# Kernel tuning notes

Measured on AMD Instinct MI355X. Metric: run time of the kernel, lower is better.

## Reference

```python
import jax, jax.numpy as jnp
import numpy as np

KD = 128   # scratch_keys_dim
NP = 3     # n_pointers
STEPS = 3  # max_program_steps


def _gru_cell(x, h, w_ih, w_hh, b_ih, b_hh):
    # torch.nn.GRUCell math
    gi = x @ w_ih.T + b_ih            # [B, 3H]
    gh = h @ w_hh.T + b_hh            # [B, 3H]
    ir, iz, inn = jnp.split(gi, 3, axis=-1)
    hr, hz, hn = jnp.split(gh, 3, axis=-1)
    r = jax.nn.sigmoid(ir + hr)
    z = jax.nn.sigmoid(iz + hz)
    n = jnp.tanh(inn + r * hn)
    return (1.0 - z) * n + z * h


def setup_inputs() -> dict:
    key = jax.random.key(0)
    ks = jax.random.split(key, 9)
    B, Lw, La, V, P, H = 256, 12, 51, 1000, 200, 3 * KD
    instructions = jax.random.randint(ks[0], (Lw, B), 0, V)
    true_actions = jax.random.randint(ks[1], (La, B), 0, V)
    gate_emb = jax.random.normal(ks[2], (V, 2)) * 0.1
    program_emb = jax.random.normal(ks[3], (V, P)) * 0.1
    primitive_emb = jax.random.normal(ks[4], (V, V)) * 0.1
    # sinusoidal positional encoding = scratch_keys buffer
    pos = np.arange(50)[:, None].astype(np.float32)
    div = np.exp(np.arange(0, KD, 2).astype(np.float32) * (-np.log(10000.0) / KD))
    pe = np.zeros((50, KD), np.float32)
    pe[:, 0::2] = np.sin(pos * div)
    pe[:, 1::2] = np.cos(pos * div)
    scratch_keys = jnp.asarray(pe)
    init_value = jnp.zeros((V,), jnp.float32).at[0].set(1.0)  # one-hot at eos_idx=0
    w_ih = jax.random.normal(ks[5], (3 * H, P)) * 0.05
    w_hh = jax.random.normal(ks[6], (3 * H, H)) * 0.05
    b_ih = jax.random.normal(ks[7], (3 * H,)) * 0.05
    b_hh = jax.random.normal(ks[8], (3 * H,)) * 0.05
    return dict(gate_emb=gate_emb, program_emb=program_emb, primitive_emb=primitive_emb,
                scratch_keys=scratch_keys, init_value=init_value,
                w_ih=w_ih, w_hh=w_hh, b_ih=b_ih, b_hh=b_hh,
                instructions=instructions, true_actions=true_actions)


def reference(gate_emb, program_emb, primitive_emb, scratch_keys, init_value,
              w_ih, w_hh, b_ih, b_hh, instructions, true_actions):
    ins = instructions[1:-1]          # drop BOS/EOS, [Lw-2, B]
    acts = true_actions[1:]           # [L, B]
    L = acts.shape[0]                 # scratch length (50)
    B = instructions.shape[1]
    V = init_value.shape[0]
    keys = scratch_keys[:L]           # [L, KD]
    h0 = jnp.tile(scratch_keys[0], (B, NP))           # [B, 3*KD]
    sv0 = jnp.tile(init_value, (B, L, 1))             # [B, L, V]

    def word_step(carry, word):
        h, sv = carry
        gate = jax.nn.softmax(gate_emb[word], axis=-1)     # [B, 2]
        program = program_emb[word]                        # [B, P]
        primitive = primitive_emb[word]                    # [B, V]
        g0 = gate[:, 0:1]
        g1 = gate[:, 1:2]
        for _ in range(STEPS):
            read_p = h[:, KD:2 * KD]
            write_p = h[:, 2 * KD:3 * KD]
            # attention read from scratch memory
            read_attn = jax.nn.softmax(read_p @ keys.T, axis=-1)      # [B, L]
            read_value = jnp.einsum('bl,blv->bv', read_attn, sv)       # [B, V]
            # gated mix of primitive embedding and read value
            new_value = g0 * primitive + g1 * read_value                # [B, V]
            # attention write
            write_mask = jax.nn.softmax(write_p @ keys.T, axis=-1)      # [B, L]
            wm = write_mask[..., None]                                  # [B, L, 1]
            sv = wm * new_value[:, None, :] + (1.0 - wm) * sv
            # gated GRU controller update
            h_new = _gru_cell(program, h, w_ih, w_hh, b_ih, b_hh)
            h = g0 * h + g1 * h_new
        return (h, sv), None

    (_, sv), _ = jax.lax.scan(word_step, (h0, sv0), ins)
    actions = jax.nn.log_softmax(sv, axis=-1)          # [B, L, V]
    actions = jnp.transpose(actions, (0, 2, 1))        # [B, V, L]
    return actions, acts.T                             # ([B,V,L], [B,L])
```

## Files before the change

### kernel.cpp

```cpp
#include <hip/hip_runtime.h>
#include <hip/hip_fp16.h>
#include <hip/hip_fp8.h>

#define B_ 256
#define V_ 1000
#define P_ 200
#define L_ 50
#define H_ 384
#define H3_ 1152
#define NW_ 10
#define OUT1_OFF 12800000

typedef _Float16 half8 __attribute__((ext_vector_type(8)));
typedef _Float16 half4_t __attribute__((ext_vector_type(4)));
typedef _Float16 half2_t __attribute__((ext_vector_type(2)));
typedef float floatx4 __attribute__((ext_vector_type(4)));

__global__ __launch_bounds__(256) void prep_kernel(
    const float* __restrict__ gate_emb, const float* __restrict__ prog_emb,
    const float* __restrict__ w_ih, const float* __restrict__ w_hh,
    const int* __restrict__ instr, const int* __restrict__ tacts,
    float* __restrict__ g01, unsigned char* __restrict__ whhP,
    unsigned char* __restrict__ whhR,
    _Float16* __restrict__ wih_h, _Float16* __restrict__ prog_h,
    float* __restrict__ out)
{
  const int stride = gridDim.x * blockDim.x;
  const int tid = blockIdx.x * blockDim.x + threadIdx.x;

  for (int i = tid; i < 147456; i += stride) {
    const int e = i & 7, p = (i >> 3) & 1, l = (i >> 4) & 63;
    const int q = i >> 10;
    const int u = q % 18, w = q / 18;
    const int g = u / 6, kap = u - 6*g;
    const int kc = 2*kap + p;
    const int row = g*384 + 48*w + 16*2 + (l & 15);
    const int col = kc*32 + (l >> 4)*8 + e;
    __hip_fp8_e4m3 qv(w_hh[row*H_ + col]);
    whhP[i] = qv.__x;
  }
  for (int i = tid; i < 294912; i += stride) {
    const int e = i & 7, p = (i >> 3) & 1, l = (i >> 4) & 63;
    const int q = i >> 10;
    const int u = q % 36, w = q / 36;
    const int j = u / 18, rem = u - 18*j;
    const int g = rem / 6, kap = rem - 6*g;
    const int kc = 2*kap + p;
    const int row = g*384 + 48*w + 16*j + (l & 15);
    const int col = kc*32 + (l >> 4)*8 + e;
    __hip_fp8_e4m3 qv(w_hh[row*H_ + col]);
    whhR[i] = qv.__x;
  }
  for (int i = tid; i < H3_*224; i += stride) {
    int r = i / 224, c = i - r*224;
    wih_h[i] = (_Float16)(c < P_ ? w_ih[r*P_ + c] : 0.f);
  }
  for (int i = tid; i < V_*P_; i += stride) prog_h[i] = (_Float16)prog_emb[i];
  for (int i = tid; i < NW_*B_; i += stride) {
    int w = i / B_, b = i - w*B_;
    int word = instr[(1+w)*B_ + b];
    float e0 = gate_emb[word*2], e1 = gate_emb[word*2+1];
    float m = fmaxf(e0, e1);
    float a = __expf(e0-m), c = __expf(e1-m);
    float inv = 1.f/(a+c);
    g01[i*2] = a*inv; g01[i*2+1] = c*inv;
  }
  for (int i = tid; i < B_*L_; i += stride) {
    int b = i / L_, l = i - b*L_;
    out[OUT1_OFF + i] = (float)tacts[(1+l)*B_ + b];
  }
}

__global__ __launch_bounds__(256) void gi_gemm(
    const _Float16* __restrict__ prog_h, const _Float16* __restrict__ wih_h,
    const float* __restrict__ b_ih, const float* __restrict__ b_hh,
    float* __restrict__ giv)
{
  __shared__ _Float16 pA[16][232];
  const int tid = threadIdx.x;
  const int v0 = blockIdx.x * 16;
  const int n0 = blockIdx.y * 64;

  for (int i = tid; i < 16*224; i += 256) {
    int r = i / 224, c = i - r*224;
    int v = v0 + r;
    _Float16 val = (_Float16)0.f;
    if (v < V_ && c < P_) val = prog_h[v*P_ + c];
    pA[r][c] = val;
  }
  __syncthreads();

  const int wave = tid >> 6, lane = tid & 63;
  const int m = lane & 15, kg = lane >> 4;
  const int n_t = n0 + wave*16;
  floatx4 acc = {0.f, 0.f, 0.f, 0.f};
  #pragma unroll
  for (int ks = 0; ks < 7; ++ks) {
    const int kk = ks*32 + kg*8;
    half8 av = *(const half8*)&pA[m][kk];
    half8 bv = *(const half8*)&wih_h[(n_t + m)*224 + kk];
    acc = __builtin_amdgcn_mfma_f32_16x16x32_f16(av, bv, acc, 0, 0, 0);
  }
  const int nn = n_t + m;
  const float bias = b_ih[nn] + (nn < 768 ? b_hh[nn] : 0.f);
  #pragma unroll
  for (int r = 0; r < 4; ++r) {
    int mm = v0 + kg*4 + r;
    if (mm < V_) giv[(size_t)mm*H3_ + nn] = acc[r] + bias;
  }
}

__global__ __launch_bounds__(512, 2) void steps_kernel(
    const uint4* __restrict__ whhPp, const uint4* __restrict__ whhRp,
    const float* __restrict__ giv, const float* __restrict__ g01,
    const float* __restrict__ keys, const float* __restrict__ bhh,
    const int* __restrict__ instr, _Float16* __restrict__ hdump)
{
  __shared__ uint4 ldsP[9216];
  __shared__ unsigned long long hA[768];

  const int bid = blockIdx.x, b0 = bid*16, tid = threadIdx.x;
  const int w = tid >> 6, lane = tid & 63, m_ = lane & 15, kg = lane >> 4;

  for (int i = tid; i < 9216; i += 512) ldsP[i] = whhPp[i];

  const uint4* __restrict__ rbase = whhRp + (size_t)w*36*64 + lane;

  float hreg[3][4];
  float bbn[3];
  half2_t gvh[18];
  float g0r[4], g1r[4];

  #pragma unroll
  for (int j = 0; j < 3; ++j) bbn[j] = bhh[768 + 48*w + 16*j + m_];

  #pragma unroll
  for (int j = 0; j < 3; ++j) {
    const float h0 = keys[(48*w + 16*j + m_) & 127];
    #pragma unroll
    for (int r = 0; r < 4; ++r) hreg[j][r] = h0;
  }

  #pragma unroll
  for (int j = 0; j < 3; ++j) {
    const int c = 48*w + 16*j + m_;
    const int base = (c >> 5)*512 + ((c >> 3) & 3)*128 + (c & 7);
    half4_t hv;
    #pragma unroll
    for (int r = 0; r < 4; ++r) {
      __hip_fp8_e4m3 q(hreg[j][r]);
      ((unsigned char*)hA)[base + (kg*4 + r)*8] = q.__x;
      hv[r] = (_Float16)hreg[j][r];
    }
    *(half4_t*)&hdump[(((size_t)0*16 + bid)*384 + c)*16 + kg*4] = hv;
  }

  {
    int4 wd4 = *(const int4*)&instr[(1+0)*B_ + b0 + kg*4];
    int wdr[4] = {wd4.x, wd4.y, wd4.z, wd4.w};
    #pragma unroll
    for (int r = 0; r < 4; ++r) {
      float2 gg = *(const float2*)&g01[(size_t)(b0 + kg*4 + r)*2];
      g0r[r] = gg.x; g1r[r] = gg.y;
    }
    #pragma unroll
    for (int r = 0; r < 4; ++r) {
      const float* gp = giv + (size_t)wdr[r]*H3_;
      #pragma unroll
      for (int j = 0; j < 3; ++j)
        #pragma unroll
        for (int g = 0; g < 3; ++g) {
          const int f = r*9 + j*3 + g;
          gvh[f >> 1][f & 1] = (_Float16)gp[g*384 + 48*w + 16*j + m_];
        }
    }
  }

  uint4 W00 = rbase[ 0*64], W01 = rbase[ 1*64], W02 = rbase[ 2*64];
  uint4 W03 = rbase[ 3*64], W04 = rbase[ 4*64], W05 = rbase[ 5*64];
  uint4 W06 = rbase[ 6*64], W07 = rbase[ 7*64], W08 = rbase[ 8*64];
  uint4 W09 = rbase[ 9*64], W10 = rbase[10*64], W11 = rbase[11*64];
  uint4 W12 = rbase[12*64], W13 = rbase[13*64], W14 = rbase[14*64];
  uint4 W15 = rbase[15*64], W16 = rbase[16*64], W17 = rbase[17*64];
  uint4 W18 = rbase[18*64], W19 = rbase[19*64], W20 = rbase[20*64];
  uint4 W21 = rbase[21*64], W22 = rbase[22*64], W23 = rbase[23*64];
  uint4 W24 = rbase[24*64], W25 = rbase[25*64], W26 = rbase[26*64];
  uint4 W27 = rbase[27*64], W28 = rbase[28*64], W29 = rbase[29*64];
  uint4 W30 = rbase[30*64], W31 = rbase[31*64], W32 = rbase[32*64];
  uint4 W33 = rbase[33*64], W34 = rbase[34*64], W35 = rbase[35*64];

#define PIN4(W) asm volatile("" : "+v"(W.x), "+v"(W.y), "+v"(W.z), "+v"(W.w))
  PIN4(W00); PIN4(W01); PIN4(W02); PIN4(W03); PIN4(W04); PIN4(W05);
  PIN4(W06); PIN4(W07); PIN4(W08); PIN4(W09); PIN4(W10); PIN4(W11);
  PIN4(W12); PIN4(W13); PIN4(W14); PIN4(W15); PIN4(W16); PIN4(W17);
  PIN4(W18); PIN4(W19); PIN4(W20); PIN4(W21); PIN4(W22); PIN4(W23);
  PIN4(W24); PIN4(W25); PIN4(W26); PIN4(W27); PIN4(W28); PIN4(W29);
  PIN4(W30); PIN4(W31); PIN4(W32); PIN4(W33); PIN4(W34); PIN4(W35);
#undef PIN4

  asm volatile("s_waitcnt lgkmcnt(0)\n\ts_barrier" ::: "memory");

#define LO64(W) ((long)((((unsigned long long)(W).y) << 32) | (W).x))
#define HI64(W) ((long)((((unsigned long long)(W).w) << 32) | (W).z))
#define GVF(F) ((float)gvh[(F) >> 1][(F) & 1])
#define KSTEP(KAP, WA, WB, WC) \
  a0 = hA[(2*(KAP))*64 + lane]; a1 = hA[(2*(KAP)+1)*64 + lane]; \
  acc0 = __builtin_amdgcn_mfma_f32_16x16x32_fp8_fp8((long)a0, LO64(WA), acc0, 0, 0, 0); \
  acc0 = __builtin_amdgcn_mfma_f32_16x16x32_fp8_fp8((long)a1, HI64(WA), acc0, 0, 0, 0); \
  acc1 = __builtin_amdgcn_mfma_f32_16x16x32_fp8_fp8((long)a0, LO64(WB), acc1, 0, 0, 0); \
  acc1 = __builtin_amdgcn_mfma_f32_16x16x32_fp8_fp8((long)a1, HI64(WB), acc1, 0, 0, 0); \
  acc2 = __builtin_amdgcn_mfma_f32_16x16x32_fp8_fp8((long)a0, LO64(WC), acc2, 0, 0, 0); \
  acc2 = __builtin_amdgcn_mfma_f32_16x16x32_fp8_fp8((long)a1, HI64(WC), acc2, 0, 0, 0);
#define KSTEPL(KAP) \
  { a0 = hA[(2*(KAP))*64 + lane]; a1 = hA[(2*(KAP)+1)*64 + lane]; \
    uint4 P0 = ldsP[(w*18 +      (KAP))*64 + lane]; \
    uint4 P1 = ldsP[(w*18 +  6 + (KAP))*64 + lane]; \
    uint4 P2 = ldsP[(w*18 + 12 + (KAP))*64 + lane]; \
    acc0 = __builtin_amdgcn_mfma_f32_16x16x32_fp8_fp8((long)a0, LO64(P0), acc0, 0, 0, 0); \
    acc0 = __builtin_amdgcn_mfma_f32_16x16x32_fp8_fp8((long)a1, HI64(P0), acc0, 0, 0, 0); \
    acc1 = __builtin_amdgcn_mfma_f32_16x16x32_fp8_fp8((long)a0, LO64(P1), acc1, 0, 0, 0); \
    acc1 = __builtin_amdgcn_mfma_f32_16x16x32_fp8_fp8((long)a1, HI64(P1), acc1, 0, 0, 0); \
    acc2 = __builtin_amdgcn_mfma_f32_16x16x32_fp8_fp8((long)a0, LO64(P2), acc2, 0, 0, 0); \
    acc2 = __builtin_amdgcn_mfma_f32_16x16x32_fp8_fp8((long)a1, HI64(P2), acc2, 0, 0, 0); }
#define EPI(J) \
  _Pragma("unroll") \
  for (int r = 0; r < 4; ++r) { \
    const float rg = 1.f/(1.f + __expf(-(GVF(r*9+(J)*3+0) + acc0[r]))); \
    const float z  = 1.f/(1.f + __expf(-(GVF(r*9+(J)*3+1) + acc1[r]))); \
    const float x2 = GVF(r*9+(J)*3+2) + rg*(acc2[r] + bbn[(J)]); \
    const float nn = 2.f/(1.f + __expf(-2.f*x2)) - 1.f; \
    const float hold = hreg[(J)][r]; \
    const float hnew = (1.f - z)*nn + z*hold; \
    hreg[(J)][r] = g0r[r]*hold + g1r[r]*hnew; \
  }

  #pragma unroll 1
  for (int t = 0; t < 30; ++t) {
    unsigned long long a0, a1;
    floatx4 acc0, acc1, acc2;

    acc0 = (floatx4){0.f,0.f,0.f,0.f}; acc1 = acc0; acc2 = acc0;
    KSTEP(0, W00, W06, W12) KSTEP(1, W01, W07, W13) KSTEP(2, W02, W08, W14)
    KSTEP(3, W03, W09, W15) KSTEP(4, W04, W10, W16) KSTEP(5, W05, W11, W17)
    EPI(0)
    acc0 = (floatx4){0.f,0.f,0.f,0.f}; acc1 = acc0; acc2 = acc0;
    KSTEP(0, W18, W24, W30) KSTEP(1, W19, W25, W31) KSTEP(2, W20, W26, W32)
    KSTEP(3, W21, W27, W33) KSTEP(4, W22, W28, W34) KSTEP(5, W23, W29, W35)
    EPI(1)
    acc0 = (floatx4){0.f,0.f,0.f,0.f}; acc1 = acc0; acc2 = acc0;
    KSTEPL(0) KSTEPL(1) KSTEPL(2) KSTEPL(3) KSTEPL(4) KSTEPL(5)
    EPI(2)

    asm volatile("s_waitcnt lgkmcnt(0)\n\ts_barrier" ::: "memory");

    #pragma unroll
    for (int j = 0; j < 3; ++j) {
      const int c = 48*w + 16*j + m_;
      const int base = (c >> 5)*512 + ((c >> 3) & 3)*128 + (c & 7);
      half4_t hv;
      #pragma unroll
      for (int r = 0; r < 4; ++r) {
        __hip_fp8_e4m3 q(hreg[j][r]);
        ((unsigned char*)hA)[base + (kg*4 + r)*8] = q.__x;
        hv[r] = (_Float16)hreg[j][r];
      }
      *(half4_t*)&hdump[(((size_t)(t+1)*16 + bid)*384 + c)*16 + kg*4] = hv;
    }

    if (t % 3 == 2) {
      const int wi = (t/3 + 1 < 10) ? t/3 + 1 : 9;
      int4 wd4 = *(const int4*)&instr[(1+wi)*B_ + b0 + kg*4];
      int wdr[4] = {wd4.x, wd4.y, wd4.z, wd4.w};
      #pragma unroll
      for (int r = 0; r < 4; ++r) {
        float2 gg = *(const float2*)&g01[((size_t)wi*B_ + b0 + kg*4 + r)*2];
        g0r[r] = gg.x; g1r[r] = gg.y;
      }
      #pragma unroll
      for (int r = 0; r < 4; ++r) {
        const float* gp = giv + (size_t)wdr[r]*H3_;
        #pragma unroll
        for (int j = 0; j < 3; ++j)
          #pragma unroll
          for (int g = 0; g < 3; ++g) {
            const int f = r*9 + j*3 + g;
            gvh[f >> 1][f & 1] = (_Float16)gp[g*384 + 48*w + 16*j + m_];
          }
      }
    }

    asm volatile("s_waitcnt lgkmcnt(0)\n\ts_barrier" ::: "memory");
  }
  asm volatile("s_waitcnt vmcnt(0) lgkmcnt(0)" ::: "memory");
#undef KSTEP
#undef KSTEPL
#undef EPI
#undef GVF
#undef LO64
#undef HI64
}

__global__ __launch_bounds__(256) void attnS_kernel(
    const _Float16* __restrict__ hdump, const float* __restrict__ keys,
    const float* __restrict__ g01, float* __restrict__ S_buf)
{
  __shared__ float keysT[128][52];
  __shared__ float hT[30][256];
  __shared__ float sc[30][2][52];
  __shared__ float Sr[50][13];
  __shared__ float g0a[10], g1a[10];
  __shared__ float nvs[12];

  const int b = blockIdx.x, g = b >> 4, bl = b & 15;
  const int tid = threadIdx.x, wv = tid >> 6, lane = tid & 63;

  for (int i = tid; i < 128*L_; i += 256) {
    int k = i / L_, l = i - k*L_;
    keysT[k][l] = keys[l*128 + k];
  }
  for (int i = tid; i < 30*256; i += 256) {
    int t = i >> 8, c = i & 255;
    hT[t][c] = (float)hdump[(((size_t)t*16 + g)*384 + 128 + c)*16 + bl];
  }
  for (int i = tid; i < 550; i += 256) Sr[i/11][i%11] = ((i % 11) == 0) ? 1.f : 0.f;
  if (tid < NW_) {
    float2 gg = *(const float2*)&g01[((size_t)tid*B_ + b)*2];
    g0a[tid] = gg.x; g1a[tid] = gg.y;
  }
  __syncthreads();

  for (int row = wv; row < 60; row += 4) {
    const int t = row >> 1, ty = row & 1;
    float s = 0.f;
    if (lane < L_) {
      #pragma unroll 8
      for (int k = 0; k < 128; ++k)
        s += hT[t][ty*128 + k] * keysT[k][lane];
    }
    float val = (lane < L_) ? s : -1e30f;
    float mx = val;
    #pragma unroll
    for (int off = 32; off; off >>= 1) mx = fmaxf(mx, __shfl_xor(mx, off));
    float e = (lane < L_) ? __expf(val - mx) : 0.f;
    float sm = e;
    #pragma unroll
    for (int off = 32; off; off >>= 1) sm += __shfl_xor(sm, off);
    if (lane < L_) sc[t][ty][lane] = e / sm;
  }
  __syncthreads();

  for (int t = 0; t < 30; ++t) {
    const int widx = t / 3;
    if (tid < 11) {
      float rv = 0.f;
      #pragma unroll 5
      for (int l = 0; l < L_; ++l) rv += sc[t][0][l] * Sr[l][tid];
      nvs[tid] = g1a[widx]*rv + ((tid == 1 + widx) ? g0a[widx] : 0.f);
    }
    __syncthreads();
    for (int i = tid; i < 550; i += 256) {
      const int l = i / 11, j = i - l*11;
      const float wm = sc[t][1][l];
      Sr[l][j] = wm*nvs[j] + (1.f - wm)*Sr[l][j];
    }
    __syncthreads();
  }

  for (int i = tid; i < 550; i += 256) {
    const int l = i / 11, j = i - l*11;
    S_buf[(size_t)b*600 + l*12 + j] = Sr[l][j];
  }
}

__global__ __launch_bounds__(512) void epi_kernel(
    const float* __restrict__ S_buf, const float* __restrict__ prim_emb,
    const float* __restrict__ iv_g, const int* __restrict__ instr,
    float* __restrict__ out)
{
  __shared__ float prim[10][1000];
  __shared__ float iv[1000];
  __shared__ float SrT[11][52];
  __shared__ float lss[52];
  __shared__ int wds[10];

  const int b = blockIdx.x;
  const int tid = threadIdx.x;

  if (tid < 10) wds[tid] = instr[(1+tid)*B_ + b];
  for (int i = tid; i < 550; i += 512) {
    int l = i / 11, j = i - l*11;
    SrT[j][l] = S_buf[(size_t)b*600 + l*12 + j];
  }
  for (int i = tid; i < 250; i += 512) ((float4*)iv)[i] = ((const float4*)iv_g)[i];
  __syncthreads();
  for (int wi = 0; wi < 10; ++wi) {
    const float4* __restrict__ src = (const float4*)(prim_emb + (size_t)wds[wi]*V_);
    for (int i = tid; i < 250; i += 512) ((float4*)prim[wi])[i] = src[i];
  }
  __syncthreads();

  const int wv = tid >> 6, lane = tid & 63;
  for (int l = wv; l < L_; l += 8) {
    float c0 = SrT[0][l];
    float cw[10];
    #pragma unroll
    for (int wi = 0; wi < 10; ++wi) cw[wi] = SrT[1+wi][l];
    float sv[16];
    float mx = -1e30f;
    #pragma unroll
    for (int jj = 0; jj < 16; ++jj) {
      int v = lane + 64*jj;
      float s = -1e30f;
      if (v < V_) {
        s = c0 * iv[v];
        #pragma unroll
        for (int wi = 0; wi < 10; ++wi) s += cw[wi]*prim[wi][v];
      }
      sv[jj] = s;
      mx = fmaxf(mx, s);
    }
    #pragma unroll
    for (int off = 32; off; off >>= 1) mx = fmaxf(mx, __shfl_xor(mx, off));
    float se = 0.f;
    #pragma unroll
    for (int jj = 0; jj < 16; ++jj) {
      int v = lane + 64*jj;
      if (v < V_) se += __expf(sv[jj] - mx);
    }
    #pragma unroll
    for (int off = 32; off; off >>= 1) se += __shfl_xor(se, off);
    if (lane == 0) lss[l] = mx + __logf(se);
  }
  __syncthreads();

  float* __restrict__ dst = out + (size_t)b*50000;
  for (int e = tid; e < 50000; e += 512) {
    const int v = e / 50, l = e - v*50;
    float s = SrT[0][l]*iv[v];
    #pragma unroll
    for (int wi = 0; wi < 10; ++wi) s += SrT[1+wi][l]*prim[wi][v];
    dst[e] = s - lss[l];
  }
}

extern "C" void kernel_launch(void* const* d_in, const int* in_sizes, int n_in,
                              void* d_out, int out_size, void* d_ws, size_t ws_size,
                              hipStream_t stream)
{
  (void)in_sizes; (void)n_in; (void)out_size; (void)ws_size;
  const float* gate_emb = (const float*)d_in[0];
  const float* prog_emb = (const float*)d_in[1];
  const float* prim_emb = (const float*)d_in[2];
  const float* sk       = (const float*)d_in[3];
  const float* iv       = (const float*)d_in[4];
  const float* w_ih     = (const float*)d_in[5];
  const float* w_hh     = (const float*)d_in[6];
  const float* b_ih     = (const float*)d_in[7];
  const float* b_hh     = (const float*)d_in[8];
  const int*   instr    = (const int*)d_in[9];
  const int*   tacts    = (const int*)d_in[10];
  float* out = (float*)d_out;

  float* ws     = (float*)d_ws;
  float* S_buf  = ws;
  float* g01    = S_buf + B_*600;
  float* giv    = g01 + NW_*B_*2;
  unsigned char* whhP = (unsigned char*)(giv + (size_t)V_*H3_);
  unsigned char* whhR = whhP + 147456;
  _Float16* wih_h  = (_Float16*)(whhR + 294912);
  _Float16* prog_h = wih_h + (size_t)H3_*224;
  _Float16* hdump  = prog_h + (size_t)V_*P_;

  hipLaunchKernelGGL(prep_kernel, dim3(1024), dim3(256), 0, stream,
      gate_emb, prog_emb, w_ih, w_hh, instr, tacts,
      g01, whhP, whhR, wih_h, prog_h, out);

  hipLaunchKernelGGL(gi_gemm, dim3(63, 18), dim3(256), 0, stream,
      prog_h, wih_h, b_ih, b_hh, giv);

  hipLaunchKernelGGL(steps_kernel, dim3(16), dim3(512), 0, stream,
      (const uint4*)whhP, (const uint4*)whhR, giv, g01, sk, b_hh, instr, hdump);

  hipLaunchKernelGGL(attnS_kernel, dim3(256), dim3(256), 0, stream,
      hdump, sk, g01, S_buf);

  hipLaunchKernelGGL(epi_kernel, dim3(256), dim3(512), 0, stream,
      S_buf, prim_emb, iv, instr, out);
}
```

Baseline: 299.2 us.

## Halve steps_kernel waves so each holds six column tiles with more register-resident weights

The recurrent steps kernel now runs 4 waves per block instead of 8, and each wave owns 96 hidden columns (6 tiles of 16) instead of 48. Each wave keeps 4 of its 6 tiles of fp8 W_hh in registers (72 uint4) and streams the other 2 from LDS, with waves_per_eu forced to 1 to allow the larger register budget. The h operand for all K chunks is preloaded once per step before a barrier rather than reread per tile. This is meant to cut per-step barrier and synchronization overhead and LDS traffic, at the cost of less parallelism per CU and a longer serial MFMA chain per wave.

```diff
diff --git a/kernel.cpp b/kernel.cpp
--- a/kernel.cpp
+++ b/kernel.cpp
@@ -31,10 +31,11 @@
   for (int i = tid; i < 147456; i += stride) {
     const int e = i & 7, p = (i >> 3) & 1, l = (i >> 4) & 63;
     const int q = i >> 10;
-    const int u = q % 18, w = q / 18;
-    const int g = u / 6, kap = u - 6*g;
+    const int v = q % 36, w = q / 36;
+    const int j = 4 + v / 18, rem = v % 18;
+    const int g = rem / 6, kap = rem - 6*g;
     const int kc = 2*kap + p;
-    const int row = g*384 + 48*w + 16*2 + (l & 15);
+    const int row = g*384 + 96*w + 16*j + (l & 15);
     const int col = kc*32 + (l >> 4)*8 + e;
     __hip_fp8_e4m3 qv(w_hh[row*H_ + col]);
     whhP[i] = qv.__x;
@@ -42,11 +43,11 @@
   for (int i = tid; i < 294912; i += stride) {
     const int e = i & 7, p = (i >> 3) & 1, l = (i >> 4) & 63;
     const int q = i >> 10;
-    const int u = q % 36, w = q / 36;
-    const int j = u / 18, rem = u - 18*j;
+    const int u = q % 72, w = q / 72;
+    const int j = u / 18, rem = u % 18;
     const int g = rem / 6, kap = rem - 6*g;
     const int kc = 2*kap + p;
-    const int row = g*384 + 48*w + 16*j + (l & 15);
+    const int row = g*384 + 96*w + 16*j + (l & 15);
     const int col = kc*32 + (l >> 4)*8 + e;
     __hip_fp8_e4m3 qv(w_hh[row*H_ + col]);
     whhR[i] = qv.__x;
@@ -110,7 +111,9 @@
   }
 }
 
-__global__ __launch_bounds__(512, 2) void steps_kernel(
+__global__ __launch_bounds__(256)
+__attribute__((amdgpu_waves_per_eu(1, 1)))
+void steps_kernel(
     const uint4* __restrict__ whhPp, const uint4* __restrict__ whhRp,
     const float* __restrict__ giv, const float* __restrict__ g01,
     const float* __restrict__ keys, const float* __restrict__ bhh,
@@ -122,28 +125,28 @@
   const int bid = blockIdx.x, b0 = bid*16, tid = threadIdx.x;
   const int w = tid >> 6, lane = tid & 63, m_ = lane & 15, kg = lane >> 4;
 
-  for (int i = tid; i < 9216; i += 512) ldsP[i] = whhPp[i];
-
-  const uint4* __restrict__ rbase = whhRp + (size_t)w*36*64 + lane;
-
-  float hreg[3][4];
-  float bbn[3];
-  half2_t gvh[18];
+  for (int i = tid; i < 9216; i += 256) ldsP[i] = whhPp[i];
+
+  const uint4* __restrict__ rbase = whhRp + (size_t)w*72*64 + lane;
+
+  float hreg[6][4];
+  float bbn[6];
+  half2_t gvh[36];
   float g0r[4], g1r[4];
 
   #pragma unroll
-  for (int j = 0; j < 3; ++j) bbn[j] = bhh[768 + 48*w + 16*j + m_];
+  for (int j = 0; j < 6; ++j) bbn[j] = bhh[768 + 96*w + 16*j + m_];
 
   #pragma unroll
-  for (int j = 0; j < 3; ++j) {
-    const float h0 = keys[(48*w + 16*j + m_) & 127];
+  for (int j = 0; j < 6; ++j) {
+    const float h0 = keys[(96*w + 16*j + m_) & 127];
     #pragma unroll
     for (int r = 0; r < 4; ++r) hreg[j][r] = h0;
   }
 
   #pragma unroll
-  for (int j = 0; j < 3; ++j) {
-    const int c = 48*w + 16*j + m_;
+  for (int j = 0; j < 6; ++j) {
+    const int c = 96*w + 16*j + m_;
     const int base = (c >> 5)*512 + ((c >> 3) & 3)*128 + (c & 7);
     half4_t hv;
     #pragma unroll
@@ -155,107 +158,112 @@
     *(half4_t*)&hdump[(((size_t)0*16 + bid)*384 + c)*16 + kg*4] = hv;
   }
 
-  {
-    int4 wd4 = *(const int4*)&instr[(1+0)*B_ + b0 + kg*4];
-    int wdr[4] = {wd4.x, wd4.y, wd4.z, wd4.w};
-    #pragma unroll
-    for (int r = 0; r < 4; ++r) {
-      float2 gg = *(const float2*)&g01[(size_t)(b0 + kg*4 + r)*2];
-      g0r[r] = gg.x; g1r[r] = gg.y;
-    }
-    #pragma unroll
-    for (int r = 0; r < 4; ++r) {
-      const float* gp = giv + (size_t)wdr[r]*H3_;
-      #pragma unroll
-      for (int j = 0; j < 3; ++j)
-        #pragma unroll
-        for (int g = 0; g < 3; ++g) {
-          const int f = r*9 + j*3 + g;
-          gvh[f >> 1][f & 1] = (_Float16)gp[g*384 + 48*w + 16*j + m_];
-        }
-    }
-  }
-
-  uint4 W00 = rbase[ 0*64], W01 = rbase[ 1*64], W02 = rbase[ 2*64];
-  uint4 W03 = rbase[ 3*64], W04 = rbase[ 4*64], W05 = rbase[ 5*64];
-  uint4 W06 = rbase[ 6*64], W07 = rbase[ 7*64], W08 = rbase[ 8*64];
-  uint4 W09 = rbase[ 9*64], W10 = rbase[10*64], W11 = rbase[11*64];
-  uint4 W12 = rbase[12*64], W13 = rbase[13*64], W14 = rbase[14*64];
-  uint4 W15 = rbase[15*64], W16 = rbase[16*64], W17 = rbase[17*64];
-  uint4 W18 = rbase[18*64], W19 = rbase[19*64], W20 = rbase[20*64];
-  uint4 W21 = rbase[21*64], W22 = rbase[22*64], W23 = rbase[23*64];
-  uint4 W24 = rbase[24*64], W25 = rbase[25*64], W26 = rbase[26*64];
-  uint4 W27 = rbase[27*64], W28 = rbase[28*64], W29 = rbase[29*64];
-  uint4 W30 = rbase[30*64], W31 = rbase[31*64], W32 = rbase[32*64];
-  uint4 W33 = rbase[33*64], W34 = rbase[34*64], W35 = rbase[35*64];
-
-#define PIN4(W) asm volatile("" : "+v"(W.x), "+v"(W.y), "+v"(W.z), "+v"(W.w))
-  PIN4(W00); PIN4(W01); PIN4(W02); PIN4(W03); PIN4(W04); PIN4(W05);
-  PIN4(W06); PIN4(W07); PIN4(W08); PIN4(W09); PIN4(W10); PIN4(W11);
-  PIN4(W12); PIN4(W13); PIN4(W14); PIN4(W15); PIN4(W16); PIN4(W17);
-  PIN4(W18); PIN4(W19); PIN4(W20); PIN4(W21); PIN4(W22); PIN4(W23);
-  PIN4(W24); PIN4(W25); PIN4(W26); PIN4(W27); PIN4(W28); PIN4(W29);
-  PIN4(W30); PIN4(W31); PIN4(W32); PIN4(W33); PIN4(W34); PIN4(W35);
-#undef PIN4
+#define LOADGI(WI) { \
+    int4 wd4_ = *(const int4*)&instr[(1+(WI))*B_ + b0 + kg*4]; \
+    int wdr_[4] = {wd4_.x, wd4_.y, wd4_.z, wd4_.w}; \
+    _Pragma("unroll") \
+    for (int r = 0; r < 4; ++r) { \
+      float2 gg_ = *(const float2*)&g01[((size_t)(WI)*B_ + b0 + kg*4 + r)*2]; \
+      g0r[r] = gg_.x; g1r[r] = gg_.y; \
+    } \
+    _Pragma("unroll") \
+    for (int r = 0; r < 4; ++r) { \
+      const float* gp_ = giv + (size_t)wdr_[r]*H3_; \
+      _Pragma("unroll") \
+      for (int j = 0; j < 6; ++j) \
+        _Pragma("unroll") \
+        for (int g = 0; g < 3; ++g) { \
+          const int f_ = (r*6 + j)*3 + g; \
+          gvh[f_ >> 1][f_ & 1] = (_Float16)gp_[g*384 + 96*w + 16*j + m_]; \
+        } \
+    } }
+
+  LOADGI(0)
+
+#define DECLU(NAME, IDX) \
+  unsigned long long NAME##L, NAME##H; \
+  { uint4 t_ = rbase[(IDX)*64]; \
+    NAME##L = (((unsigned long long)t_.y) << 32) | t_.x; \
+    NAME##H = (((unsigned long long)t_.w) << 32) | t_.z; }
+#define DECLJ(J) \
+  DECLU(W##J##g0k0, (J)*18+ 0) DECLU(W##J##g0k1, (J)*18+ 1) DECLU(W##J##g0k2, (J)*18+ 2) \
+  DECLU(W##J##g0k3, (J)*18+ 3) DECLU(W##J##g0k4, (J)*18+ 4) DECLU(W##J##g0k5, (J)*18+ 5) \
+  DECLU(W##J##g1k0, (J)*18+ 6) DECLU(W##J##g1k1, (J)*18+ 7) DECLU(W##J##g1k2, (J)*18+ 8) \
+  DECLU(W##J##g1k3, (J)*18+ 9) DECLU(W##J##g1k4, (J)*18+10) DECLU(W##J##g1k5, (J)*18+11) \
+  DECLU(W##J##g2k0, (J)*18+12) DECLU(W##J##g2k1, (J)*18+13) DECLU(W##J##g2k2, (J)*18+14) \
+  DECLU(W##J##g2k3, (J)*18+15) DECLU(W##J##g2k4, (J)*18+16) DECLU(W##J##g2k5, (J)*18+17)
+
+  DECLJ(0) DECLJ(1) DECLJ(2) DECLJ(3)
+
+#define PINU(NAME) asm volatile("" : "+v"(NAME##L), "+v"(NAME##H));
+#define PINJ(J) \
+  PINU(W##J##g0k0) PINU(W##J##g0k1) PINU(W##J##g0k2) PINU(W##J##g0k3) PINU(W##J##g0k4) PINU(W##J##g0k5) \
+  PINU(W##J##g1k0) PINU(W##J##g1k1) PINU(W##J##g1k2) PINU(W##J##g1k3) PINU(W##J##g1k4) PINU(W##J##g1k5) \
+  PINU(W##J##g2k0) PINU(W##J##g2k1) PINU(W##J##g2k2) PINU(W##J##g2k3) PINU(W##J##g2k4) PINU(W##J##g2k5)
+
+  PINJ(0) PINJ(1) PINJ(2) PINJ(3)
 
   asm volatile("s_waitcnt lgkmcnt(0)\n\ts_barrier" ::: "memory");
 
-#define LO64(W) ((long)((((unsigned long long)(W).y) << 32) | (W).x))
-#define HI64(W) ((long)((((unsigned long long)(W).w) << 32) | (W).z))
+#define MFMA_(ACC, A, B) \
+  ACC = __builtin_amdgcn_mfma_f32_16x16x32_fp8_fp8((long)(A), (long)(B), ACC, 0, 0, 0)
+#define Z4 ((floatx4){0.f, 0.f, 0.f, 0.f})
 #define GVF(F) ((float)gvh[(F) >> 1][(F) & 1])
-#define KSTEP(KAP, WA, WB, WC) \
-  a0 = hA[(2*(KAP))*64 + lane]; a1 = hA[(2*(KAP)+1)*64 + lane]; \
-  acc0 = __builtin_amdgcn_mfma_f32_16x16x32_fp8_fp8((long)a0, LO64(WA), acc0, 0, 0, 0); \
-  acc0 = __builtin_amdgcn_mfma_f32_16x16x32_fp8_fp8((long)a1, HI64(WA), acc0, 0, 0, 0); \
-  acc1 = __builtin_amdgcn_mfma_f32_16x16x32_fp8_fp8((long)a0, LO64(WB), acc1, 0, 0, 0); \
-  acc1 = __builtin_amdgcn_mfma_f32_16x16x32_fp8_fp8((long)a1, HI64(WB), acc1, 0, 0, 0); \
-  acc2 = __builtin_amdgcn_mfma_f32_16x16x32_fp8_fp8((long)a0, LO64(WC), acc2, 0, 0, 0); \
-  acc2 = __builtin_amdgcn_mfma_f32_16x16x32_fp8_fp8((long)a1, HI64(WC), acc2, 0, 0, 0);
-#define KSTEPL(KAP) \
-  { a0 = hA[(2*(KAP))*64 + lane]; a1 = hA[(2*(KAP)+1)*64 + lane]; \
-    uint4 P0 = ldsP[(w*18 +      (KAP))*64 + lane]; \
-    uint4 P1 = ldsP[(w*18 +  6 + (KAP))*64 + lane]; \
-    uint4 P2 = ldsP[(w*18 + 12 + (KAP))*64 + lane]; \
-    acc0 = __builtin_amdgcn_mfma_f32_16x16x32_fp8_fp8((long)a0, LO64(P0), acc0, 0, 0, 0); \
-    acc0 = __builtin_amdgcn_mfma_f32_16x16x32_fp8_fp8((long)a1, HI64(P0), acc0, 0, 0, 0); \
-    acc1 = __builtin_amdgcn_mfma_f32_16x16x32_fp8_fp8((long)a0, LO64(P1), acc1, 0, 0, 0); \
-    acc1 = __builtin_amdgcn_mfma_f32_16x16x32_fp8_fp8((long)a1, HI64(P1), acc1, 0, 0, 0); \
-    acc2 = __builtin_amdgcn_mfma_f32_16x16x32_fp8_fp8((long)a0, LO64(P2), acc2, 0, 0, 0); \
-    acc2 = __builtin_amdgcn_mfma_f32_16x16x32_fp8_fp8((long)a1, HI64(P2), acc2, 0, 0, 0); }
+#define KAP6(K, R, Zw, N) \
+  MFMA_(acc0, av[2*(K)],   R##L); \
+  MFMA_(acc1, av[2*(K)],   Zw##L); \
+  MFMA_(acc2, av[2*(K)],   N##L); \
+  MFMA_(acc0, av[2*(K)+1], R##H); \
+  MFMA_(acc1, av[2*(K)+1], Zw##H); \
+  MFMA_(acc2, av[2*(K)+1], N##H);
+#define KAPL(J, K) { \
+  uint4 P0 = ldsP[(w*36 + ((J)-4)*18 +      (K))*64 + lane]; \
+  uint4 P1 = ldsP[(w*36 + ((J)-4)*18 +  6 + (K))*64 + lane]; \
+  uint4 P2 = ldsP[(w*36 + ((J)-4)*18 + 12 + (K))*64 + lane]; \
+  MFMA_(acc0, av[2*(K)],   (((unsigned long long)P0.y) << 32) | P0.x); \
+  MFMA_(acc1, av[2*(K)],   (((unsigned long long)P1.y) << 32) | P1.x); \
+  MFMA_(acc2, av[2*(K)],   (((unsigned long long)P2.y) << 32) | P2.x); \
+  MFMA_(acc0, av[2*(K)+1], (((unsigned long long)P0.w) << 32) | P0.z); \
+  MFMA_(acc1, av[2*(K)+1], (((unsigned long long)P1.w) << 32) | P1.z); \
+  MFMA_(acc2, av[2*(K)+1], (((unsigned long long)P2.w) << 32) | P2.z); }
 #define EPI(J) \
   _Pragma("unroll") \
   for (int r = 0; r < 4; ++r) { \
-    const float rg = 1.f/(1.f + __expf(-(GVF(r*9+(J)*3+0) + acc0[r]))); \
-    const float z  = 1.f/(1.f + __expf(-(GVF(r*9+(J)*3+1) + acc1[r]))); \
-    const float x2 = GVF(r*9+(J)*3+2) + rg*(acc2[r] + bbn[(J)]); \
+    const float rg = 1.f/(1.f + __expf(-(GVF((r*6+(J))*3+0) + acc0[r]))); \
+    const float z  = 1.f/(1.f + __expf(-(GVF((r*6+(J))*3+1) + acc1[r]))); \
+    const float x2 = GVF((r*6+(J))*3+2) + rg*(acc2[r] + bbn[(J)]); \
     const float nn = 2.f/(1.f + __expf(-2.f*x2)) - 1.f; \
     const float hold = hreg[(J)][r]; \
     const float hnew = (1.f - z)*nn + z*hold; \
     hreg[(J)][r] = g0r[r]*hold + g1r[r]*hnew; \
   }
+#define JREG(J) \
+  acc0 = Z4; acc1 = Z4; acc2 = Z4; \
+  KAP6(0, W##J##g0k0, W##J##g1k0, W##J##g2k0) \
+  KAP6(1, W##J##g0k1, W##J##g1k1, W##J##g2k1) \
+  KAP6(2, W##J##g0k2, W##J##g1k2, W##J##g2k2) \
+  KAP6(3, W##J##g0k3, W##J##g1k3, W##J##g2k3) \
+  KAP6(4, W##J##g0k4, W##J##g1k4, W##J##g2k4) \
+  KAP6(5, W##J##g0k5, W##J##g1k5, W##J##g2k5) \
+  EPI(J)
+#define JLDS(J) \
+  acc0 = Z4; acc1 = Z4; acc2 = Z4; \
+  KAPL(J, 0) KAPL(J, 1) KAPL(J, 2) KAPL(J, 3) KAPL(J, 4) KAPL(J, 5) \
+  EPI(J)
 
   #pragma unroll 1
   for (int t = 0; t < 30; ++t) {
-    unsigned long long a0, a1;
+    unsigned long long av[12];
+    #pragma unroll
+    for (int kc = 0; kc < 12; ++kc) av[kc] = hA[kc*64 + lane];
+    asm volatile("s_waitcnt lgkmcnt(0)\n\ts_barrier" ::: "memory");
+
     floatx4 acc0, acc1, acc2;
-
-    acc0 = (floatx4){0.f,0.f,0.f,0.f}; acc1 = acc0; acc2 = acc0;
-    KSTEP(0, W00, W06, W12) KSTEP(1, W01, W07, W13) KSTEP(2, W02, W08, W14)
-    KSTEP(3, W03, W09, W15) KSTEP(4, W04, W10, W16) KSTEP(5, W05, W11, W17)
-    EPI(0)
-    acc0 = (floatx4){0.f,0.f,0.f,0.f}; acc1 = acc0; acc2 = acc0;
-    KSTEP(0, W18, W24, W30) KSTEP(1, W19, W25, W31) KSTEP(2, W20, W26, W32)
-    KSTEP(3, W21, W27, W33) KSTEP(4, W22, W28, W34) KSTEP(5, W23, W29, W35)
-    EPI(1)
-    acc0 = (floatx4){0.f,0.f,0.f,0.f}; acc1 = acc0; acc2 = acc0;
-    KSTEPL(0) KSTEPL(1) KSTEPL(2) KSTEPL(3) KSTEPL(4) KSTEPL(5)
-    EPI(2)
-
-    asm volatile("s_waitcnt lgkmcnt(0)\n\ts_barrier" ::: "memory");
-
-    #pragma unroll
-    for (int j = 0; j < 3; ++j) {
-      const int c = 48*w + 16*j + m_;
+    JREG(0) JREG(1) JREG(2) JREG(3) JLDS(4) JLDS(5)
+
+    #pragma unroll
+    for (int j = 0; j < 6; ++j) {
+      const int c = 96*w + 16*j + m_;
       const int base = (c >> 5)*512 + ((c >> 3) & 3)*128 + (c & 7);
       half4_t hv;
       #pragma unroll
@@ -269,35 +277,25 @@
 
     if (t % 3 == 2) {
       const int wi = (t/3 + 1 < 10) ? t/3 + 1 : 9;
-      int4 wd4 = *(const int4*)&instr[(1+wi)*B_ + b0 + kg*4];
-      int wdr[4] = {wd4.x, wd4.y, wd4.z, wd4.w};
-      #pragma unroll
-      for (int r = 0; r < 4; ++r) {
-        float2 gg = *(const float2*)&g01[((size_t)wi*B_ + b0 + kg*4 + r)*2];
-        g0r[r] = gg.x; g1r[r] = gg.y;
-      }
-      #pragma unroll
-      for (int r = 0; r < 4; ++r) {
-        const float* gp = giv + (size_t)wdr[r]*H3_;
-        #pragma unroll
-        for (int j = 0; j < 3; ++j)
-          #pragma unroll
-          for (int g = 0; g < 3; ++g) {
-            const int f = r*9 + j*3 + g;
-            gvh[f >> 1][f & 1] = (_Float16)gp[g*384 + 48*w + 16*j + m_];
-          }
-      }
+      LOADGI(wi)
     }
 
     asm volatile("s_waitcnt lgkmcnt(0)\n\ts_barrier" ::: "memory");
   }
   asm volatile("s_waitcnt vmcnt(0) lgkmcnt(0)" ::: "memory");
-#undef KSTEP
-#undef KSTEPL
+#undef JREG
+#undef JLDS
+#undef KAP6
+#undef KAPL
 #undef EPI
 #undef GVF
-#undef LO64
-#undef HI64
+#undef Z4
+#undef MFMA_
+#undef PINJ
+#undef PINU
+#undef DECLJ
+#undef DECLU
+#undef LOADGI
 }
 
 __global__ __launch_bounds__(256) void attnS_kernel(
@@ -478,7 +476,7 @@
   hipLaunchKernelGGL(gi_gemm, dim3(63, 18), dim3(256), 0, stream,
       prog_h, wih_h, b_ih, b_hh, giv);
 
-  hipLaunchKernelGGL(steps_kernel, dim3(16), dim3(512), 0, stream,
+  hipLaunchKernelGGL(steps_kernel, dim3(16), dim3(256), 0, stream,
       (const uint4*)whhP, (const uint4*)whhR, giv, g01, sk, b_hh, instr, hdump);
 
   hipLaunchKernelGGL(attnS_kernel, dim3(256), dim3(256), 0, stream,
```

Result: slower. 403.1 us (+34.7%).
